# Kernel tuning notes

Measured on AMD Instinct MI355X. Metric: run time of the kernel, lower is better.

The kernel has to match this reference:

```python
import jax, jax.numpy as jnp
import numpy as np

NUM_HEADS = 16


def setup_inputs() -> dict:
    B, S, A, H = 2, 2048, 16, 1024
    key = jax.random.key(0)
    k1, k2, k3, k4, k5, k6 = jax.random.split(key, 6)
    h1 = jax.random.normal(k1, (B, S, H), dtype=jnp.float32)
    h2 = jax.random.normal(k2, (B, A, H), dtype=jnp.float32)
    # variable-length boolean masks (at least one valid position per row)
    sent_len = jax.random.randint(k3, (B,), S // 2, S + 1)
    sentence_mask = jnp.arange(S)[None, :] < sent_len[:, None]
    asp_len = jax.random.randint(k4, (B,), 1, A + 1)
    aspect_mask = jnp.arange(A)[None, :] < asp_len[:, None]
    # xavier-uniform-ish init for Linear weights stored torch-style [out, in]
    bound = float(np.sqrt(6.0 / (H + H)))
    Wq = jax.random.uniform(k5, (H, H), jnp.float32, -bound, bound)
    Wk = jax.random.uniform(k6, (H, H), jnp.float32, -bound, bound)
    return {"h1": h1, "h2": h2, "sentence_mask": sentence_mask,
            "aspect_mask": aspect_mask, "Wq": Wq, "Wk": Wk}


def reference(h1, h2, sentence_mask, aspect_mask, Wq, Wk):
    B, S, H = h1.shape
    hd = H // NUM_HEADS
    scale = hd ** -0.5

    # --- masked mean aggregation of aspect features: [B, A, H] -> [B, H] ---
    m = aspect_mask.astype(h2.dtype)                      # [B, A]
    lengths = jnp.clip(m.sum(axis=1, keepdims=True), 1.0)  # [B, 1]
    h2_agg = (h2 * m[..., None]).sum(axis=1) / lengths     # [B, H]

    # query = aggregated aspect broadcast over seq positions: [B, S, H]
    h3 = jnp.broadcast_to(h2_agg[:, None, :], (B, S, H))

    # Linear (no bias), torch convention y = x @ W^T
    Q = jnp.einsum('bsh,oh->bso', h3, Wq)                  # [B, S, H]
    K = jnp.einsum('bsh,oh->bso', h1, Wk)                  # [B, S, H]

    Qh = Q.reshape(B, S, NUM_HEADS, hd)                    # [B, S, nh, hd]
    Kh = K.reshape(B, S, NUM_HEADS, hd)

    # scaled dot-product scores: [B, nh, S, S]
    scores = jnp.einsum('bqhd,bkhd->bhqk', Qh, Kh) * scale

    # key-side mask: broadcast [B, S] over (heads, query) dims
    scores = jnp.where(sentence_mask[:, None, None, :], scores, -jnp.inf)

    weights = jax.nn.softmax(scores, axis=-1)              # [B, nh, S, S]
    attention_matrix = weights.mean(axis=1)                # [B, S, S]
    return attention_matrix
```

## Files before the change

kernel.cpp:

```cpp
#include <hip/hip_runtime.h>

#define B 2
#define S 2048
#define A 16
#define H 1024
#define NH 16
#define HD 64
#define KT 8
#define HG 8
#define CH 4
#define QC 16
#define KC 1024

__global__ __launch_bounds__(256) void kQW(const float* __restrict__ h2,
                                           const int* __restrict__ amask,
                                           const float* __restrict__ Wq,
                                           const float* __restrict__ Wk,
                                           float* __restrict__ weff) {
    __shared__ float agg[H];
    __shared__ float qs[HD];
    int blk = blockIdx.x;
    int c = blk & (CH - 1);
    int bh = blk / CH;
    int b = bh >> 4, h = bh & 15;
    int tid = threadIdx.x;

    {
        const float4* h2b = (const float4*)(h2 + (size_t)b * A * H);
        float4 sum = make_float4(0.f, 0.f, 0.f, 0.f);
        int cnt = 0;
#pragma unroll
        for (int a = 0; a < A; a++) {
            if (amask[b * A + a]) {
                float4 v = h2b[a * (H / 4) + tid];
                sum.x += v.x; sum.y += v.y; sum.z += v.z; sum.w += v.w; cnt++;
            }
        }
        float inv = 1.0f / (float)(cnt > 0 ? cnt : 1);
        ((float4*)agg)[tid] = make_float4(sum.x * inv, sum.y * inv, sum.z * inv, sum.w * inv);
    }
    __syncthreads();

    int wave = tid >> 6, lane = tid & 63;
    const float4* ag = (const float4*)agg;
    for (int d = wave * 16; d < wave * 16 + 16; d++) {
        const float4* wr = (const float4*)(Wq + (size_t)(h * HD + d) * H);
        float acc = 0.f;
#pragma unroll
        for (int t = 0; t < 4; t++) {
            int j4 = lane + 64 * t;
            float4 a4 = ag[j4], w4 = wr[j4];
            acc += a4.x * w4.x + a4.y * w4.y + a4.z * w4.z + a4.w * w4.w;
        }
        for (int off = 32; off > 0; off >>= 1) acc += __shfl_down(acc, off);
        if (lane == 0) qs[d] = acc;
    }
    __syncthreads();

    int j = c * 256 + tid;
    float acc = 0.f;
#pragma unroll 8
    for (int d = 0; d < HD; d++) acc += qs[d] * Wk[(size_t)(h * HD + d) * H + j];
    weff[((size_t)b * NH + h) * H + j] = acc * 0.125f;
}

__global__ __launch_bounds__(256) void kB(const float* __restrict__ h1,
                                          const float* __restrict__ weff,
                                          float* __restrict__ s) {
    __shared__ float4 lw[HG * H / 4];
    int blk = blockIdx.x;
    int hg = blk & 1;
    int rest = blk >> 1;
    int kt = rest % (S / KT);
    int b  = rest / (S / KT);
    const float4* wsrc = (const float4*)(weff + ((size_t)b * NH + hg * HG) * H);
    for (int i = threadIdx.x; i < HG * H / 4; i += 256) lw[i] = wsrc[i];
    __syncthreads();

    int wave = threadIdx.x >> 6, lane = threadIdx.x & 63;
    for (int kl = wave; kl < KT; kl += 4) {
        int k = kt * KT + kl;
        const float4* row = (const float4*)(h1 + ((size_t)b * S + k) * H);
        float4 x[4];
#pragma unroll
        for (int t = 0; t < 4; t++) x[t] = row[lane + 64 * t];
#pragma unroll
        for (int hh = 0; hh < HG; hh++) {
            float acc = 0.f;
#pragma unroll
            for (int t = 0; t < 4; t++) {
                float4 wv = lw[hh * (H / 4) + lane + 64 * t];
                acc += wv.x * x[t].x + wv.y * x[t].y + wv.z * x[t].z + wv.w * x[t].w;
            }
            for (int off = 32; off > 0; off >>= 1) acc += __shfl_down(acc, off);
            if (lane == 0) s[((size_t)b * NH + hg * HG + hh) * S + k] = acc;
        }
    }
}

__global__ __launch_bounds__(256) void kS(const float* __restrict__ s,
                                          const int* __restrict__ smask,
                                          float* __restrict__ m,
                                          float* __restrict__ dsum) {
    __shared__ float red[4];
    int bh = blockIdx.x, b = bh >> 4;
    int tid = threadIdx.x, wave = tid >> 6, lane = tid & 63;
    const float4* srow = (const float4*)(s + (size_t)bh * S);
    const int4* mrow = (const int4*)(smask + b * S);

    float mx = -3.4e38f;
#pragma unroll
    for (int t = 0; t < 2; t++) {
        int i = tid + 256 * t;
        float4 v = srow[i]; int4 mk = mrow[i];
        if (mk.x) mx = fmaxf(mx, v.x);
        if (mk.y) mx = fmaxf(mx, v.y);
        if (mk.z) mx = fmaxf(mx, v.z);
        if (mk.w) mx = fmaxf(mx, v.w);
    }
    for (int off = 32; off > 0; off >>= 1) mx = fmaxf(mx, __shfl_down(mx, off));
    if (lane == 0) red[wave] = mx;
    __syncthreads();
    float gmax = fmaxf(fmaxf(red[0], red[1]), fmaxf(red[2], red[3]));
    __syncthreads();

    float sum = 0.f;
#pragma unroll
    for (int t = 0; t < 2; t++) {
        int i = tid + 256 * t;
        float4 v = srow[i]; int4 mk = mrow[i];
        if (mk.x) sum += expf(v.x - gmax);
        if (mk.y) sum += expf(v.y - gmax);
        if (mk.z) sum += expf(v.z - gmax);
        if (mk.w) sum += expf(v.w - gmax);
    }
    for (int off = 32; off > 0; off >>= 1) sum += __shfl_down(sum, off);
    if (lane == 0) red[wave] = sum;
    __syncthreads();
    if (tid == 0) { m[bh] = gmax; dsum[bh] = red[0] + red[1] + red[2] + red[3]; }
}

__global__ __launch_bounds__(256) void kD(const float* __restrict__ s,
                                          const int* __restrict__ smask,
                                          const float* __restrict__ m,
                                          const float* __restrict__ dsum,
                                          float* __restrict__ out) {
    __shared__ float wch[KC];
    int blk = blockIdx.x;
    int b  = blk >> 8;
    int r  = blk & 255;
    int kc = r >> 7;
    int q0 = (r & 127) * QC;
    int tid = threadIdx.x;

    float mh[NH], ih[NH];
#pragma unroll
    for (int h = 0; h < NH; h++) {
        mh[h] = m[b * NH + h];
        ih[h] = 1.0f / dsum[b * NH + h];
    }

    {
        int k = kc * KC + tid * 4;
        int4 mk = *(const int4*)(smask + b * S + k);
        float4 val = make_float4(0.f, 0.f, 0.f, 0.f);
#pragma unroll
        for (int h = 0; h < NH; h++) {
            float4 sv = *(const float4*)(s + ((size_t)b * NH + h) * S + k);
            val.x += expf(sv.x - mh[h]) * ih[h];
            val.y += expf(sv.y - mh[h]) * ih[h];
            val.z += expf(sv.z - mh[h]) * ih[h];
            val.w += expf(sv.w - mh[h]) * ih[h];
        }
        const float inh = 1.0f / NH;
        val.x = mk.x ? val.x * inh : 0.f;
        val.y = mk.y ? val.y * inh : 0.f;
        val.z = mk.z ? val.z * inh : 0.f;
        val.w = mk.w ? val.w * inh : 0.f;
        ((float4*)wch)[tid] = val;
    }
    __syncthreads();

    float4 v = ((float4*)wch)[tid];
#pragma unroll
    for (int qi = 0; qi < QC; qi++) {
        float4* dst = (float4*)(out + ((size_t)(b * S + q0 + qi)) * S + kc * KC);
        dst[tid] = v;
    }
}

extern "C" void kernel_launch(void* const* d_in, const int* in_sizes, int n_in,
                              void* d_out, int out_size, void* d_ws, size_t ws_size,
                              hipStream_t stream) {
    const float* h1    = (const float*)d_in[0];
    const float* h2    = (const float*)d_in[1];
    const int*   smask = (const int*)d_in[2];
    const int*   amask = (const int*)d_in[3];
    const float* Wq    = (const float*)d_in[4];
    const float* Wk    = (const float*)d_in[5];
    float* out = (float*)d_out;
    float* ws  = (float*)d_ws;

    float* weff = ws;
    float* s    = ws + 32768;
    float* m    = ws + 98304;
    float* dsum = ws + 98336;

    kQW<<<B * NH * CH, 256, 0, stream>>>(h2, amask, Wq, Wk, weff);
    kB <<<B * (S / KT) * 2, 256, 0, stream>>>(h1, weff, s);
    kS <<<B * NH, 256, 0, stream>>>(s, smask, m, dsum);
    kD <<<B * (S / KC) * (S / QC), 256, 0, stream>>>(s, smask, m, dsum, out);
}
```

Baseline: 120.4 us.

## Fuse softmax stats into broadcast-write kernel and double kB key tile

Merges the per-head max/sum kernel and the output-writing kernel into one kernel, where every block recomputes the softmax statistics for all 16 heads of its batch from the 2048-wide score rows. This removes one launch and the global round trip for the stats, at the cost of redundant statistic computation across 128 blocks per batch. Each block now covers the full key width for its 16 query rows. The kB key tile is also doubled from 8 to 16 rows per block, which halves the block count and the weight reloads into shared memory.

```diff
diff --git a/kernel.cpp b/kernel.cpp
--- a/kernel.cpp
+++ b/kernel.cpp
@@ -6,11 +6,10 @@
 #define H 1024
 #define NH 16
 #define HD 64
-#define KT 8
+#define KT 16
 #define HG 8
 #define CH 4
 #define QC 16
-#define KC 1024
 
 __global__ __launch_bounds__(256) void kQW(const float* __restrict__ h2,
                                            const int* __restrict__ amask,
@@ -98,94 +97,87 @@
     }
 }
 
-__global__ __launch_bounds__(256) void kS(const float* __restrict__ s,
-                                          const int* __restrict__ smask,
-                                          float* __restrict__ m,
-                                          float* __restrict__ dsum) {
-    __shared__ float red[4];
-    int bh = blockIdx.x, b = bh >> 4;
+__global__ __launch_bounds__(256) void kSD(const float* __restrict__ s,
+                                           const int* __restrict__ smask,
+                                           float* __restrict__ out) {
+    __shared__ float mh[NH], ih[NH];
+    __shared__ int   mk[S];
+    __shared__ float wch[S];
+    int blk = blockIdx.x;
+    int b  = blk >> 7;
+    int q0 = (blk & 127) * QC;
     int tid = threadIdx.x, wave = tid >> 6, lane = tid & 63;
-    const float4* srow = (const float4*)(s + (size_t)bh * S);
-    const int4* mrow = (const int4*)(smask + b * S);
-
-    float mx = -3.4e38f;
+
+    {
+        const int4* msrc = (const int4*)(smask + b * S);
+#pragma unroll
+        for (int t = 0; t < 2; t++) ((int4*)mk)[tid + 256 * t] = msrc[tid + 256 * t];
+    }
+    __syncthreads();
+
+#pragma unroll
+    for (int hh = 0; hh < 4; hh++) {
+        int h = wave * 4 + hh;
+        const float4* srow = (const float4*)(s + ((size_t)b * NH + h) * S);
+        float mx = -3.4e38f;
+#pragma unroll
+        for (int t = 0; t < 8; t++) {
+            int i = lane + 64 * t;
+            float4 v = srow[i]; int4 mm = ((const int4*)mk)[i];
+            if (mm.x) mx = fmaxf(mx, v.x);
+            if (mm.y) mx = fmaxf(mx, v.y);
+            if (mm.z) mx = fmaxf(mx, v.z);
+            if (mm.w) mx = fmaxf(mx, v.w);
+        }
+        for (int off = 32; off > 0; off >>= 1) mx = fmaxf(mx, __shfl_down(mx, off));
+        mx = __shfl(mx, 0);
+        float sum = 0.f;
+#pragma unroll
+        for (int t = 0; t < 8; t++) {
+            int i = lane + 64 * t;
+            float4 v = srow[i]; int4 mm = ((const int4*)mk)[i];
+            if (mm.x) sum += expf(v.x - mx);
+            if (mm.y) sum += expf(v.y - mx);
+            if (mm.z) sum += expf(v.z - mx);
+            if (mm.w) sum += expf(v.w - mx);
+        }
+        for (int off = 32; off > 0; off >>= 1) sum += __shfl_down(sum, off);
+        if (lane == 0) { mh[h] = mx; ih[h] = 1.0f / sum; }
+    }
+    __syncthreads();
+
+    float lm[NH], li[NH];
+#pragma unroll
+    for (int h = 0; h < NH; h++) { lm[h] = mh[h]; li[h] = ih[h]; }
 #pragma unroll
     for (int t = 0; t < 2; t++) {
         int i = tid + 256 * t;
-        float4 v = srow[i]; int4 mk = mrow[i];
-        if (mk.x) mx = fmaxf(mx, v.x);
-        if (mk.y) mx = fmaxf(mx, v.y);
-        if (mk.z) mx = fmaxf(mx, v.z);
-        if (mk.w) mx = fmaxf(mx, v.w);
-    }
-    for (int off = 32; off > 0; off >>= 1) mx = fmaxf(mx, __shfl_down(mx, off));
-    if (lane == 0) red[wave] = mx;
-    __syncthreads();
-    float gmax = fmaxf(fmaxf(red[0], red[1]), fmaxf(red[2], red[3]));
-    __syncthreads();
-
-    float sum = 0.f;
-#pragma unroll
-    for (int t = 0; t < 2; t++) {
-        int i = tid + 256 * t;
-        float4 v = srow[i]; int4 mk = mrow[i];
-        if (mk.x) sum += expf(v.x - gmax);
-        if (mk.y) sum += expf(v.y - gmax);
-        if (mk.z) sum += expf(v.z - gmax);
-        if (mk.w) sum += expf(v.w - gmax);
-    }
-    for (int off = 32; off > 0; off >>= 1) sum += __shfl_down(sum, off);
-    if (lane == 0) red[wave] = sum;
-    __syncthreads();
-    if (tid == 0) { m[bh] = gmax; dsum[bh] = red[0] + red[1] + red[2] + red[3]; }
-}
-
-__global__ __launch_bounds__(256) void kD(const float* __restrict__ s,
-                                          const int* __restrict__ smask,
-                                          const float* __restrict__ m,
-                                          const float* __restrict__ dsum,
-                                          float* __restrict__ out) {
-    __shared__ float wch[KC];
-    int blk = blockIdx.x;
-    int b  = blk >> 8;
-    int r  = blk & 255;
-    int kc = r >> 7;
-    int q0 = (r & 127) * QC;
-    int tid = threadIdx.x;
-
-    float mh[NH], ih[NH];
-#pragma unroll
-    for (int h = 0; h < NH; h++) {
-        mh[h] = m[b * NH + h];
-        ih[h] = 1.0f / dsum[b * NH + h];
-    }
-
-    {
-        int k = kc * KC + tid * 4;
-        int4 mk = *(const int4*)(smask + b * S + k);
+        int4 mm = ((const int4*)mk)[i];
         float4 val = make_float4(0.f, 0.f, 0.f, 0.f);
 #pragma unroll
         for (int h = 0; h < NH; h++) {
-            float4 sv = *(const float4*)(s + ((size_t)b * NH + h) * S + k);
-            val.x += expf(sv.x - mh[h]) * ih[h];
-            val.y += expf(sv.y - mh[h]) * ih[h];
-            val.z += expf(sv.z - mh[h]) * ih[h];
-            val.w += expf(sv.w - mh[h]) * ih[h];
+            float4 sv = ((const float4*)(s + ((size_t)b * NH + h) * S))[i];
+            val.x += expf(sv.x - lm[h]) * li[h];
+            val.y += expf(sv.y - lm[h]) * li[h];
+            val.z += expf(sv.z - lm[h]) * li[h];
+            val.w += expf(sv.w - lm[h]) * li[h];
         }
         const float inh = 1.0f / NH;
-        val.x = mk.x ? val.x * inh : 0.f;
-        val.y = mk.y ? val.y * inh : 0.f;
-        val.z = mk.z ? val.z * inh : 0.f;
-        val.w = mk.w ? val.w * inh : 0.f;
-        ((float4*)wch)[tid] = val;
-    }
-    __syncthreads();
-
-    float4 v = ((float4*)wch)[tid];
+        val.x = mm.x ? val.x * inh : 0.f;
+        val.y = mm.y ? val.y * inh : 0.f;
+        val.z = mm.z ? val.z * inh : 0.f;
+        val.w = mm.w ? val.w * inh : 0.f;
+        ((float4*)wch)[i] = val;
+    }
+    __syncthreads();
+
+    float4 v0 = ((float4*)wch)[tid];
+    float4 v1 = ((float4*)wch)[tid + 256];
 #pragma unroll
     for (int qi = 0; qi < QC; qi++) {
-        float4* dst = (float4*)(out + ((size_t)(b * S + q0 + qi)) * S + kc * KC);
-        dst[tid] = v;
+        float4* dst = (float4*)(out + ((size_t)(b * S + q0 + qi)) * S);
+        dst[tid] = v0;
+        dst[tid + 256] = v1;
     }
 }
 
@@ -203,11 +195,8 @@
 
     float* weff = ws;
     float* s    = ws + 32768;
-    float* m    = ws + 98304;
-    float* dsum = ws + 98336;
 
     kQW<<<B * NH * CH, 256, 0, stream>>>(h2, amask, Wq, Wk, weff);
     kB <<<B * (S / KT) * 2, 256, 0, stream>>>(h1, weff, s);
-    kS <<<B * NH, 256, 0, stream>>>(s, smask, m, dsum);
-    kD <<<B * (S / KC) * (S / QC), 256, 0, stream>>>(s, smask, m, dsum, out);
-}
+    kSD<<<B * (S / QC), 256, 0, stream>>>(s, smask, out);
+}
```

After: 135.0 us. +12.1%, slower.
